# Kernel optimization log

Hardware: AMD Instinct MI355X
Metric: run time of the kernel (lower is better)

## Reference

```python
import jax, jax.numpy as jnp
from jax import lax
import numpy as np

PN_FEAT = 64


def _conv(x, w, b):
    # x: [B,H,W,Cin], w: [kh,kw,Cin,Cout] (SAME padding, stride 1)
    return lax.conv_general_dilated(x, w, (1, 1), 'SAME',
                                    dimension_numbers=('NHWC', 'HWIO', 'NHWC')) + b


def setup_inputs() -> dict:
    key = jax.random.key(0)
    ks = jax.random.split(key, 12)
    B, P, N, C = 4, 5000, 100, 8
    nx = ny = 240
    pillars = jax.random.normal(ks[0], (B, P, N, C), dtype=jnp.float32)
    pillar_idxs = jax.random.randint(ks[1], (B, P, 2), 0, nx).astype(jnp.int32)
    def lin(k, fi, fo):
        return jax.random.normal(k, (fi, fo), dtype=jnp.float32) / np.sqrt(fi).astype(np.float32)
    def cnv(k, kh, kw, ci, co):
        return jax.random.normal(k, (kh, kw, ci, co), dtype=jnp.float32) / np.sqrt(kh * kw * ci).astype(np.float32)
    return {
        'pillars': pillars,
        'pillar_idxs': pillar_idxs,
        'nx': nx,
        'ny': ny,
        # pointnet MLP: 8 -> 64 (tanh) -> 64
        'pn_w0': lin(ks[2], 8, 64), 'pn_b0': jnp.zeros((64,), jnp.float32),
        'pn_w1': lin(ks[3], 64, PN_FEAT), 'pn_b1': jnp.zeros((PN_FEAT,), jnp.float32),
        # resnet costmap CNN: 64 -> 128 (tanh) -> 128 (tanh) -> 1, relu output
        'cw0': cnv(ks[4], 3, 3, PN_FEAT, 128), 'cb0': jnp.zeros((128,), jnp.float32),
        'cw1': cnv(ks[5], 3, 3, 128, 128), 'cb1': jnp.zeros((128,), jnp.float32),
        'cw2': cnv(ks[6], 1, 1, 128, 1), 'cb2': jnp.zeros((1,), jnp.float32),
    }


def reference(pillars, pillar_idxs, nx, ny,
              pn_w0, pn_b0, pn_w1, pn_b1,
              cw0, cb0, cw1, cb1, cw2, cb2):
    VALID_THRESH = 1000000.0
    ACT_SCALE = 1.0
    # mask padded points (norm >= 1e6 means invalid)
    valid = (jnp.linalg.norm(pillars, axis=-1, keepdims=True) < VALID_THRESH).astype(pillars.dtype)
    # per-point MLP: [B,P,N,8] -> [B,P,N,F]
    h = jnp.tanh(pillars @ pn_w0 + pn_b0)
    feat = h @ pn_w1 + pn_b1
    # masked max over points in each pillar -> [B,P,F]
    pmax = jnp.max(feat * valid, axis=-2)
    # scatter pillar features into BEV pseudo-image [B,nx,ny,F]
    B = pillars.shape[0]
    bidx = jnp.arange(B)[:, None]                      # [B,1]
    img = jnp.zeros((B, nx, ny, PN_FEAT), pillars.dtype)
    img = img.at[bidx, pillar_idxs[..., 0], pillar_idxs[..., 1]].set(pmax)
    # costmap CNN head (NHWC internally; original is NCHW, same math)
    x = jnp.tanh(_conv(img, cw0, cb0))
    x = jnp.tanh(_conv(x, cw1, cb1))
    x = _conv(x, cw2, cb2)
    return jax.nn.relu(x) * ACT_SCALE            # [B,nx,ny,1]
```

## Files before the change

### kernel.cpp

```cpp
#include <hip/hip_runtime.h>
#include <hip/hip_bf16.h>
#include <math.h>

#define B  4
#define P  5000
#define NPT 100
#define F  64
#define NX 240
#define NY 240
#define C1 128

typedef __attribute__((ext_vector_type(8)))  short short8;
typedef __attribute__((ext_vector_type(16))) float f32x16;

__device__ __forceinline__ float tanh_fast(float x) {
    float e = exp2f(x * 2.8853900817779268f);
    float r = __builtin_amdgcn_rcpf(e + 1.0f);
    return __builtin_fmaf(-2.0f, r, 1.0f);
}
__device__ __forceinline__ short bf16_bits(float f) {
    return (short)(__bfloat16_as_ushort(__float2bfloat16(f)));
}
__device__ __forceinline__ void async_load16(const void* g, void* l) {
    __builtin_amdgcn_global_load_lds(
        (const __attribute__((address_space(1))) void*)g,
        (__attribute__((address_space(3))) void*)l, 16, 0, 0);
}

__global__ __launch_bounds__(128, 2) void pn_mfma_kernel(
    const float* __restrict__ pillars,
    const short* __restrict__ w0p,
    const __hip_bfloat16* __restrict__ w1t,
    const float* __restrict__ b1,
    const int* __restrict__ idxs,
    const int* __restrict__ winner,
    __hip_bfloat16* __restrict__ img)
{
    constexpr int XS = 40;
    __shared__ short xA[128 * XS];
    __shared__ float red[2][F];
    __shared__ unsigned int vb32[4];

    int bp = blockIdx.x;
    int n  = threadIdx.x;
    int wave = n >> 6, lane = n & 63;
    int mr = lane & 31;
    int g  = lane >> 5;
    bool live = (n < NPT);

    const float* xp = pillars + ((size_t)bp * NPT + (live ? n : 0)) * 8;
    float4 q0 = *(const float4*)xp;
    float4 q1 = *(const float4*)(xp + 4);
    float x[8] = {q0.x, q0.y, q0.z, q0.w, q1.x, q1.y, q1.z, q1.w};

    float ss = 0.f;
#pragma unroll
    for (int c = 0; c < 8; c++) ss += x[c] * x[c];
    bool valid = live && (ss < 1e12f);

    unsigned long long bal = __ballot(valid);
    if (lane == 0) {
        vb32[wave * 2]     = (unsigned)bal;
        vb32[wave * 2 + 1] = (unsigned)(bal >> 32);
    }

    short8 xhi, xlo, xone;
#pragma unroll
    for (int c = 0; c < 8; c++) {
        __hip_bfloat16 hb = __float2bfloat16(x[c]);
        float hv = __bfloat162float(hb);
        xhi[c] = (short)__bfloat16_as_ushort(hb);
        xlo[c] = bf16_bits(x[c] - hv);
        xone[c] = (c < 2) ? bf16_bits(1.0f) : (short)0;
    }
    *(short8*)&xA[n * XS + 0]  = xhi;
    *(short8*)&xA[n * XS + 8]  = xlo;
    *(short8*)&xA[n * XS + 16] = xhi;
    *(short8*)&xA[n * XS + 24] = xone;
    __syncthreads();

    short8 wb[2][2];
#pragma unroll
    for (int kk = 0; kk < 2; kk++)
#pragma unroll
        for (int m = 0; m < 2; m++)
            wb[kk][m] = *(const short8*)(w0p + ((kk * 2 + g) * 64 + m * 32 + mr) * 8);

    f32x16 acc1[2][2];
#pragma unroll
    for (int ptt = 0; ptt < 2; ptt++)
#pragma unroll
        for (int m = 0; m < 2; m++)
            acc1[ptt][m] = (f32x16){0,0,0,0,0,0,0,0,0,0,0,0,0,0,0,0};

#pragma unroll
    for (int kk = 0; kk < 2; kk++) {
        short8 x0 = *(const short8*)&xA[(wave * 64 + mr) * XS + kk * 16 + g * 8];
        short8 x1 = *(const short8*)&xA[(wave * 64 + 32 + mr) * XS + kk * 16 + g * 8];
        acc1[0][0] = __builtin_amdgcn_mfma_f32_32x32x16_bf16(wb[kk][0], x0, acc1[0][0], 0, 0, 0);
        acc1[0][1] = __builtin_amdgcn_mfma_f32_32x32x16_bf16(wb[kk][1], x0, acc1[0][1], 0, 0, 0);
        acc1[1][0] = __builtin_amdgcn_mfma_f32_32x32x16_bf16(wb[kk][0], x1, acc1[1][0], 0, 0, 0);
        acc1[1][1] = __builtin_amdgcn_mfma_f32_32x32x16_bf16(wb[kk][1], x1, acc1[1][1], 0, 0, 0);
    }

    short8 afrag[2][4];
#pragma unroll
    for (int ptt = 0; ptt < 2; ptt++) {
#pragma unroll
        for (int c0 = 0; c0 < 4; c0++) {
            short8 t;
#pragma unroll
            for (int j = 0; j < 8; j++) {
                float v = (c0 >> 1) ? acc1[ptt][1][8 * (c0 & 1) + j]
                                    : acc1[ptt][0][8 * (c0 & 1) + j];
                t[j] = bf16_bits(tanh_fast(v));
            }
            afrag[ptt][c0] = t;
        }
    }

    short8 bfrag[2][4];
#pragma unroll
    for (int nt = 0; nt < 2; nt++)
#pragma unroll
        for (int c0 = 0; c0 < 4; c0++)
            bfrag[nt][c0] = *(const short8*)((const short*)w1t +
                                (nt * 32 + mr) * F + c0 * 16 + g * 8);

    f32x16 a2[2][2];
#pragma unroll
    for (int ptt = 0; ptt < 2; ptt++)
#pragma unroll
        for (int nt = 0; nt < 2; nt++)
            a2[ptt][nt] = (f32x16){0,0,0,0,0,0,0,0,0,0,0,0,0,0,0,0};

#pragma unroll
    for (int c0 = 0; c0 < 4; c0++) {
        a2[0][0] = __builtin_amdgcn_mfma_f32_32x32x16_bf16(afrag[0][c0], bfrag[0][c0], a2[0][0], 0, 0, 0);
        a2[0][1] = __builtin_amdgcn_mfma_f32_32x32x16_bf16(afrag[0][c0], bfrag[1][c0], a2[0][1], 0, 0, 0);
        a2[1][0] = __builtin_amdgcn_mfma_f32_32x32x16_bf16(afrag[1][c0], bfrag[0][c0], a2[1][0], 0, 0, 0);
        a2[1][1] = __builtin_amdgcn_mfma_f32_32x32x16_bf16(afrag[1][c0], bfrag[1][c0], a2[1][1], 0, 0, 0);
    }

    float bv0 = b1[mr];
    float bv1 = b1[32 + mr];
    bool allv = ((vb32[0] & vb32[1] & vb32[2]) == 0xFFFFFFFFu) &&
                ((vb32[3] & 0xFu) == 0xFu);
    float mx0 = -INFINITY, mx1 = -INFINITY;

    if (allv) {
#pragma unroll
        for (int ptt = 0; ptt < 2; ptt++) {
#pragma unroll
            for (int r = 0; r < 16; r++) {
                bool inc = !(wave == 1 && ptt == 1) || (g == 0 && r < 4);
                if (inc) {
                    mx0 = fmaxf(mx0, (ptt == 0) ? a2[0][0][r] : a2[1][0][r]);
                    mx1 = fmaxf(mx1, (ptt == 0) ? a2[0][1][r] : a2[1][1][r]);
                }
            }
        }
        mx0 += bv0;
        mx1 += bv1;
    } else {
        unsigned wm0 = vb32[wave * 2];
        unsigned wm1 = vb32[wave * 2 + 1];
#pragma unroll
        for (int ptt = 0; ptt < 2; ptt++) {
            unsigned wm = (ptt == 0) ? wm0 : wm1;
#pragma unroll
            for (int r = 0; r < 16; r++) {
                int idx = (r & 3) + 8 * (r >> 2) + 4 * g;
                bool inc = !(wave == 1 && ptt == 1) || (idx < 4);
                if (inc) {
                    bool vbit = (wm >> idx) & 1;
                    float a0 = (ptt == 0) ? a2[0][0][r] : a2[1][0][r];
                    float a1 = (ptt == 0) ? a2[0][1][r] : a2[1][1][r];
                    mx0 = fmaxf(mx0, vbit ? (a0 + bv0) : 0.0f);
                    mx1 = fmaxf(mx1, vbit ? (a1 + bv1) : 0.0f);
                }
            }
        }
    }
    mx0 = fmaxf(mx0, __shfl_xor(mx0, 32, 64));
    mx1 = fmaxf(mx1, __shfl_xor(mx1, 32, 64));
    if (lane < 32) { red[wave][mr] = mx0; red[wave][32 + mr] = mx1; }
    __syncthreads();
    if (n < F) {
        float v = fmaxf(red[0][n], red[1][n]);
        int ix = idxs[bp * 2], iy = idxs[bp * 2 + 1];
        int b = bp / P, p = bp % P;
        int cell = (b * NX + ix) * NY + iy;
        if (winner[cell] == p)
            img[(size_t)cell * F + n] = __float2bfloat16(v);
    }
}

__global__ __launch_bounds__(256) void winner_kernel(
    const int* __restrict__ idxs, int* __restrict__ winner)
{
    int i = blockIdx.x * 256 + threadIdx.x;
    if (i >= B * P) return;
    int ix = idxs[i * 2], iy = idxs[i * 2 + 1];
    int b = i / P, p = i % P;
    atomicMax(&winner[(b * NX + ix) * NY + iy], p);
}

__global__ __launch_bounds__(256) void cvt_w_kernel(
    const float* __restrict__ w, __hip_bfloat16* __restrict__ wt, int cin)
{
    int idx = blockIdx.x * 256 + threadIdx.x;
    int total = 9 * cin * 128;
    if (idx >= total) return;
    int co = idx % 128;
    int rest = idx / 128;
    int ci = rest % cin;
    int t  = rest / cin;
    int c0 = ci >> 4, c16 = ci & 15;
    wt[(((size_t)(t * (cin >> 4) + c0)) * 128 + co) * 16 + c16] = __float2bfloat16(w[idx]);
}

__global__ __launch_bounds__(256) void cvt_w1_kernel(
    const float* __restrict__ w1, __hip_bfloat16* __restrict__ w1t)
{
    int idx = blockIdx.x * 256 + threadIdx.x;
    if (idx >= F * F) return;
    int nn = idx >> 6, kk = idx & 63;
    int c0 = kk >> 4, g = (kk >> 3) & 1, j = kk & 7;
    int k = 16 * c0 + 4 * g + (j & 3) + 8 * (j >> 2);
    w1t[nn * F + kk] = __float2bfloat16(w1[k * F + nn]);
}

__global__ __launch_bounds__(256) void cvt_w0p_kernel(
    const float* __restrict__ w0, const float* __restrict__ b0,
    short* __restrict__ w0p)
{
    int idx = blockIdx.x * 256 + threadIdx.x;
    if (idx >= 4 * 64 * 8) return;
    int j = idx & 7;
    int nn = (idx >> 3) & 63;
    int s = idx >> 9;
    short out = 0;
    if (s < 3) {
        float wv = w0[j * F + nn];
        __hip_bfloat16 hb = __float2bfloat16(wv);
        if (s < 2)      out = (short)__bfloat16_as_ushort(hb);
        else            out = bf16_bits(wv - __bfloat162float(hb));
    } else {
        float bv = b0[nn];
        __hip_bfloat16 hb = __float2bfloat16(bv);
        if (j == 0)      out = (short)__bfloat16_as_ushort(hb);
        else if (j == 1) out = bf16_bits(bv - __bfloat162float(hb));
    }
    w0p[idx] = out;
}

template<int CIN, bool FUSE>
__global__ __launch_bounds__(512, 2) void conv_mfma(
    const __hip_bfloat16* __restrict__ in,
    const __hip_bfloat16* __restrict__ wt,
    const float* __restrict__ bias,
    const float* __restrict__ w2,
    const float* __restrict__ b2,
    const __hip_bfloat16* __restrict__ zerobuf,
    __hip_bfloat16* __restrict__ out_bf,
    float* __restrict__ out_f)
{
    constexpr int NPASS = CIN / 32;
    constexpr int NC16  = 2;
    constexpr int CSTR  = 400;
    __shared__ short sP[2][4 * CSTR * 8];
    __shared__ float sred[FUSE ? 2 : 1][4][64];

    int tid  = threadIdx.x;
    int wave = tid >> 6;
    int lane = tid & 63;
    int mr = lane & 31;
    int g  = lane >> 5;
    int coh = wave & 1;
    int xr  = wave >> 1;
    int x0 = blockIdx.x * 4;
    int y0 = blockIdx.y * 62;
    if (y0 > 178) y0 = 178;
    int b  = blockIdx.z;
    int n0 = coh * 64;

    const short* wts = (const short*)wt;

    auto stage = [&](int pp, short* dst) {
        int gy = y0 - 1 + lane;
        bool yok = (gy >= 0 && gy < NY);
#pragma unroll
        for (int j = 0; j < 3; j++) {
            int q  = j * 8 + wave;
            int cc = q & 3;
            int dx = q >> 2;
            int gx = x0 - 1 + dx;
            const __hip_bfloat16* src =
                (yok && gx >= 0 && gx < NX)
                ? &in[(((size_t)b * NX + gx) * NY + gy) * CIN + pp * 32 + cc * 8]
                : zerobuf;
            async_load16(src, (void*)(dst + (cc * CSTR + dx * 64) * 8));
        }
    };

    f32x16 acc[2][2];
#pragma unroll
    for (int mt = 0; mt < 2; mt++)
#pragma unroll
        for (int nt = 0; nt < 2; nt++)
            acc[mt][nt] = (f32x16){0,0,0,0,0,0,0,0,0,0,0,0,0,0,0,0};

    stage(0, sP[0]);

#pragma unroll
    for (int p = 0; p < NPASS; p++) {
        __syncthreads();
        if (p + 1 < NPASS)
            stage(p + 1, sP[(p + 1) & 1]);
        const short* sPb = sP[p & 1];

#pragma unroll
        for (int tap = 0; tap < 9; tap++) {
            int kh = tap / 3, kw = tap % 3;
            int rowcol = (xr + kh) * 64 + kw;
            const short* wrow = wts + ((size_t)(tap * (CIN / 16) + p * NC16) * 128 + n0 + mr) * 16 + g * 8;
#pragma unroll
            for (int c0 = 0; c0 < NC16; c0++) {
                short8 w0f = *(const short8*)(wrow + (size_t)c0 * 2048);
                short8 w1f = *(const short8*)(wrow + (size_t)c0 * 2048 + 512);
                int cc = c0 * 2 + g;
                const short* abase = sPb + (cc * CSTR + rowcol + mr) * 8;
                short8 a0 = *(const short8*)(abase);
                short8 a1 = *(const short8*)(abase + 32 * 8);
                acc[0][0] = __builtin_amdgcn_mfma_f32_32x32x16_bf16(a0, w0f, acc[0][0], 0, 0, 0);
                acc[0][1] = __builtin_amdgcn_mfma_f32_32x32x16_bf16(a0, w1f, acc[0][1], 0, 0, 0);
                acc[1][0] = __builtin_amdgcn_mfma_f32_32x32x16_bf16(a1, w0f, acc[1][0], 0, 0, 0);
                acc[1][1] = __builtin_amdgcn_mfma_f32_32x32x16_bf16(a1, w1f, acc[1][1], 0, 0, 0);
            }
        }
    }

    float bv0 = bias[n0 + mr];
    float bv1 = bias[n0 + 32 + mr];
    if (!FUSE) {
        size_t base = ((size_t)b * NX + (x0 + xr)) * NY;
#pragma unroll
        for (int mt = 0; mt < 2; mt++) {
#pragma unroll
            for (int r = 0; r < 16; r++) {
                int row = mt * 32 + (r & 3) + 8 * (r >> 2) + 4 * g;
                if (row < 62) {
                    int y = y0 + row;
                    out_bf[(base + y) * C1 + n0 + mr]      = __float2bfloat16(tanh_fast(acc[mt][0][r] + bv0));
                    out_bf[(base + y) * C1 + n0 + 32 + mr] = __float2bfloat16(tanh_fast(acc[mt][1][r] + bv1));
                }
            }
        }
    } else {
        float w20 = w2[n0 + mr];
        float w21 = w2[n0 + 32 + mr];
#pragma unroll
        for (int mt = 0; mt < 2; mt++) {
#pragma unroll
            for (int r = 0; r < 16; r++) {
                float v = tanh_fast(acc[mt][0][r] + bv0) * w20
                        + tanh_fast(acc[mt][1][r] + bv1) * w21;
                v += __shfl_xor(v, 1, 64);
                v += __shfl_xor(v, 2, 64);
                v += __shfl_xor(v, 4, 64);
                v += __shfl_xor(v, 8, 64);
                v += __shfl_xor(v, 16, 64);
                if (mr == 0)
                    sred[coh][xr][mt * 32 + (r & 3) + 8 * (r >> 2) + 4 * g] = v;
            }
        }
        __syncthreads();
        if (tid < 256) {
            int xr2 = tid >> 6;
            int yy  = tid & 63;
            if (yy < 62) {
                float r = sred[0][xr2][yy] + sred[1][xr2][yy] + b2[0];
                out_f[((size_t)b * NX + (x0 + xr2)) * NY + (y0 + yy)] = fmaxf(r, 0.f);
            }
        }
    }
}

extern "C" void kernel_launch(void* const* d_in, const int* in_sizes, int n_in,
                              void* d_out, int out_size, void* d_ws, size_t ws_size,
                              hipStream_t stream) {
    const float* pillars = (const float*)d_in[0];
    const int*   idxs    = (const int*)d_in[1];
    const float* pn_w0   = (const float*)d_in[4];
    const float* pn_b0   = (const float*)d_in[5];
    const float* pn_w1   = (const float*)d_in[6];
    const float* pn_b1   = (const float*)d_in[7];
    const float* cw0     = (const float*)d_in[8];
    const float* cb0     = (const float*)d_in[9];
    const float* cw1     = (const float*)d_in[10];
    const float* cb1     = (const float*)d_in[11];
    const float* cw2     = (const float*)d_in[12];
    const float* cb2     = (const float*)d_in[13];
    float* out = (float*)d_out;

    char* ws = (char*)d_ws;
    const size_t IMG_BYTES  = (size_t)B * NX * NY * F * 2;
    const size_t OUT1_BYTES = (size_t)B * NX * NY * C1 * 2;
    const size_t WIN_BYTES  = (size_t)B * NX * NY * 4;
    const size_t PMAX_BYTES = (size_t)B * P * F * 4;
    const size_t WT1_BYTES  = (size_t)9 * C1 * F * 2;
    const size_t WT2_BYTES  = (size_t)9 * C1 * C1 * 2;
    const size_t W1T_BYTES  = (size_t)F * F * 2;
    const size_t W0P_BYTES  = (size_t)4 * 64 * 8 * 2;
    __hip_bfloat16* img  = (__hip_bfloat16*)ws;
    __hip_bfloat16* out1 = (__hip_bfloat16*)(ws + IMG_BYTES);
    int*   winner = (int*)(ws + IMG_BYTES + OUT1_BYTES);
    __hip_bfloat16* wt1 = (__hip_bfloat16*)(ws + IMG_BYTES + OUT1_BYTES + WIN_BYTES + PMAX_BYTES);
    __hip_bfloat16* wt2 = (__hip_bfloat16*)(ws + IMG_BYTES + OUT1_BYTES + WIN_BYTES + PMAX_BYTES + WT1_BYTES);
    __hip_bfloat16* w1t = (__hip_bfloat16*)(ws + IMG_BYTES + OUT1_BYTES + WIN_BYTES + PMAX_BYTES + WT1_BYTES + WT2_BYTES);
    short* w0p = (short*)(ws + IMG_BYTES + OUT1_BYTES + WIN_BYTES + PMAX_BYTES + WT1_BYTES + WT2_BYTES + W1T_BYTES);
    __hip_bfloat16* zerobuf = (__hip_bfloat16*)(ws + IMG_BYTES + OUT1_BYTES + WIN_BYTES + PMAX_BYTES + WT1_BYTES + WT2_BYTES + W1T_BYTES + W0P_BYTES);

    hipMemsetAsync(img, 0, IMG_BYTES, stream);
    hipMemsetAsync(winner, 0xFF, WIN_BYTES, stream);
    hipMemsetAsync(zerobuf, 0, 64, stream);

    cvt_w_kernel<<<(9 * F * C1 + 255) / 256, 256, 0, stream>>>(cw0, wt1, F);
    cvt_w_kernel<<<(9 * C1 * C1 + 255) / 256, 256, 0, stream>>>(cw1, wt2, C1);
    cvt_w1_kernel<<<(F * F + 255) / 256, 256, 0, stream>>>(pn_w1, w1t);
    cvt_w0p_kernel<<<(4 * 64 * 8 + 255) / 256, 256, 0, stream>>>(pn_w0, pn_b0, w0p);

    winner_kernel<<<(B * P + 255) / 256, 256, 0, stream>>>(idxs, winner);
    pn_mfma_kernel<<<B * P, 128, 0, stream>>>(pillars, w0p, w1t, pn_b1,
                                              idxs, winner, img);

    conv_mfma<F, false><<<dim3(NX / 4, 4, B), 512, 0, stream>>>(
        img, wt1, cb0, nullptr, nullptr, zerobuf, out1, nullptr);
    conv_mfma<C1, true><<<dim3(NX / 4, 4, B), 512, 0, stream>>>(
        out1, wt2, cb1, cw2, cb2, zerobuf, nullptr, out);
}
```

Measured before the change: 325.1 us.

## Pad conv activations with y-halo and read A operands directly from global

Stores the BEV image and first conv output with a zero-padded y dimension (248 rows, one halo row before the data), so the convolution kernels no longer need boundary checks in y. The LDS staging with async global-to-LDS loads and the per-pass barriers are removed; each lane instead precomputes nine tap offsets and loads its MFMA A fragments straight from global memory, with out-of-range x rows redirected to a zeroed pad buffer. A small halo kernel zeroes the padding rows of the intermediate buffer. This trades shared-memory reuse across taps for more global/L2 traffic, relying on cache hits to avoid the sync and staging cost.

New measurement: 501.2 us. 1.54x slower.

```diff
diff --git a/kernel.cpp b/kernel.cpp
--- a/kernel.cpp
+++ b/kernel.cpp
@@ -9,6 +9,7 @@
 #define NX 240
 #define NY 240
 #define C1 128
+#define YP 248
 
 typedef __attribute__((ext_vector_type(8)))  short short8;
 typedef __attribute__((ext_vector_type(16))) float f32x16;
@@ -20,11 +21,6 @@
 }
 __device__ __forceinline__ short bf16_bits(float f) {
     return (short)(__bfloat16_as_ushort(__float2bfloat16(f)));
-}
-__device__ __forceinline__ void async_load16(const void* g, void* l) {
-    __builtin_amdgcn_global_load_lds(
-        (const __attribute__((address_space(1))) void*)g,
-        (__attribute__((address_space(3))) void*)l, 16, 0, 0);
 }
 
 __global__ __launch_bounds__(128, 2) void pn_mfma_kernel(
@@ -190,9 +186,8 @@
         float v = fmaxf(red[0][n], red[1][n]);
         int ix = idxs[bp * 2], iy = idxs[bp * 2 + 1];
         int b = bp / P, p = bp % P;
-        int cell = (b * NX + ix) * NY + iy;
-        if (winner[cell] == p)
-            img[(size_t)cell * F + n] = __float2bfloat16(v);
+        if (winner[(b * NX + ix) * NY + iy] == p)
+            img[((size_t)(b * NX + ix) * YP + iy + 1) * F + n] = __float2bfloat16(v);
     }
 }
 
@@ -204,6 +199,20 @@
     int ix = idxs[i * 2], iy = idxs[i * 2 + 1];
     int b = i / P, p = i % P;
     atomicMax(&winner[(b * NX + ix) * NY + iy], p);
+}
+
+__global__ __launch_bounds__(256) void halo_kernel(__hip_bfloat16* __restrict__ out1)
+{
+    int idx = blockIdx.x * 256 + threadIdx.x;
+    if (idx >= B * NX * 4 * (C1 / 8)) return;
+    int c8   = idx & 15;
+    int rest = idx >> 4;
+    int rowi = rest & 3;
+    int rest2 = rest >> 2;
+    int x = rest2 % NX, b = rest2 / NX;
+    int yi = (rowi == 0) ? 0 : (240 + rowi);
+    short8 z = {0,0,0,0,0,0,0,0};
+    *(short8*)&out1[(((size_t)(b * NX + x)) * YP + yi) * C1 + c8 * 8] = z;
 }
 
 __global__ __launch_bounds__(256) void cvt_w_kernel(
@@ -262,14 +271,11 @@
     const float* __restrict__ bias,
     const float* __restrict__ w2,
     const float* __restrict__ b2,
-    const __hip_bfloat16* __restrict__ zerobuf,
+    int zoff,
     __hip_bfloat16* __restrict__ out_bf,
     float* __restrict__ out_f)
 {
     constexpr int NPASS = CIN / 32;
-    constexpr int NC16  = 2;
-    constexpr int CSTR  = 400;
-    __shared__ short sP[2][4 * CSTR * 8];
     __shared__ float sred[FUSE ? 2 : 1][4][64];
 
     int tid  = threadIdx.x;
@@ -285,24 +291,25 @@
     int b  = blockIdx.z;
     int n0 = coh * 64;
 
+    const short* inp = (const short*)in;
     const short* wts = (const short*)wt;
 
-    auto stage = [&](int pp, short* dst) {
-        int gy = y0 - 1 + lane;
-        bool yok = (gy >= 0 && gy < NY);
-#pragma unroll
-        for (int j = 0; j < 3; j++) {
-            int q  = j * 8 + wave;
-            int cc = q & 3;
-            int dx = q >> 2;
-            int gx = x0 - 1 + dx;
-            const __hip_bfloat16* src =
-                (yok && gx >= 0 && gx < NX)
-                ? &in[(((size_t)b * NX + gx) * NY + gy) * CIN + pp * 32 + cc * 8]
-                : zerobuf;
-            async_load16(src, (void*)(dst + (cc * CSTR + dx * 64) * 8));
-        }
-    };
+    int voff[3][3][2];
+#pragma unroll
+    for (int kh = 0; kh < 3; kh++) {
+        int gx = x0 - 1 + xr + kh;
+        bool xok = (gx >= 0 && gx < NX);
+#pragma unroll
+        for (int kw = 0; kw < 3; kw++)
+#pragma unroll
+            for (int mt = 0; mt < 2; mt++) {
+                int yi = y0 + kw + mr + 32 * mt;
+                voff[kh][kw][mt] = xok
+                    ? (((b * NX + gx) * YP + yi) * CIN + g * 8)
+                    : (zoff + lane * 8);
+            }
+    }
+    int wlane = (n0 + mr) * 16 + g * 8;
 
     f32x16 acc[2][2];
 #pragma unroll
@@ -311,28 +318,19 @@
         for (int nt = 0; nt < 2; nt++)
             acc[mt][nt] = (f32x16){0,0,0,0,0,0,0,0,0,0,0,0,0,0,0,0};
 
-    stage(0, sP[0]);
-
 #pragma unroll
     for (int p = 0; p < NPASS; p++) {
-        __syncthreads();
-        if (p + 1 < NPASS)
-            stage(p + 1, sP[(p + 1) & 1]);
-        const short* sPb = sP[p & 1];
-
 #pragma unroll
         for (int tap = 0; tap < 9; tap++) {
-            int kh = tap / 3, kw = tap % 3;
-            int rowcol = (xr + kh) * 64 + kw;
-            const short* wrow = wts + ((size_t)(tap * (CIN / 16) + p * NC16) * 128 + n0 + mr) * 16 + g * 8;
-#pragma unroll
-            for (int c0 = 0; c0 < NC16; c0++) {
-                short8 w0f = *(const short8*)(wrow + (size_t)c0 * 2048);
-                short8 w1f = *(const short8*)(wrow + (size_t)c0 * 2048 + 512);
-                int cc = c0 * 2 + g;
-                const short* abase = sPb + (cc * CSTR + rowcol + mr) * 8;
-                short8 a0 = *(const short8*)(abase);
-                short8 a1 = *(const short8*)(abase + 32 * 8);
+            const int kh = tap / 3, kw = tap % 3;
+#pragma unroll
+            for (int c0 = 0; c0 < 2; c0++) {
+                const int wu  = (tap * (CIN / 16) + p * 2 + c0) * 2048;
+                const int cio = p * 32 + c0 * 16;
+                short8 w0f = *(const short8*)(wts + wu + wlane);
+                short8 w1f = *(const short8*)(wts + wu + wlane + 512);
+                short8 a0  = *(const short8*)(inp + voff[kh][kw][0] + cio);
+                short8 a1  = *(const short8*)(inp + voff[kh][kw][1] + cio);
                 acc[0][0] = __builtin_amdgcn_mfma_f32_32x32x16_bf16(a0, w0f, acc[0][0], 0, 0, 0);
                 acc[0][1] = __builtin_amdgcn_mfma_f32_32x32x16_bf16(a0, w1f, acc[0][1], 0, 0, 0);
                 acc[1][0] = __builtin_amdgcn_mfma_f32_32x32x16_bf16(a1, w0f, acc[1][0], 0, 0, 0);
@@ -344,16 +342,16 @@
     float bv0 = bias[n0 + mr];
     float bv1 = bias[n0 + 32 + mr];
     if (!FUSE) {
-        size_t base = ((size_t)b * NX + (x0 + xr)) * NY;
+        size_t base = ((size_t)b * NX + (x0 + xr)) * YP;
 #pragma unroll
         for (int mt = 0; mt < 2; mt++) {
 #pragma unroll
             for (int r = 0; r < 16; r++) {
                 int row = mt * 32 + (r & 3) + 8 * (r >> 2) + 4 * g;
                 if (row < 62) {
-                    int y = y0 + row;
-                    out_bf[(base + y) * C1 + n0 + mr]      = __float2bfloat16(tanh_fast(acc[mt][0][r] + bv0));
-                    out_bf[(base + y) * C1 + n0 + 32 + mr] = __float2bfloat16(tanh_fast(acc[mt][1][r] + bv1));
+                    int yi = y0 + row + 1;
+                    out_bf[(base + yi) * C1 + n0 + mr]      = __float2bfloat16(tanh_fast(acc[mt][0][r] + bv0));
+                    out_bf[(base + yi) * C1 + n0 + 32 + mr] = __float2bfloat16(tanh_fast(acc[mt][1][r] + bv1));
                 }
             }
         }
@@ -405,10 +403,9 @@
     float* out = (float*)d_out;
 
     char* ws = (char*)d_ws;
-    const size_t IMG_BYTES  = (size_t)B * NX * NY * F * 2;
-    const size_t OUT1_BYTES = (size_t)B * NX * NY * C1 * 2;
+    const size_t IMG_BYTES  = (size_t)B * NX * YP * F * 2;
+    const size_t OUT1_BYTES = (size_t)B * NX * YP * C1 * 2;
     const size_t WIN_BYTES  = (size_t)B * NX * NY * 4;
-    const size_t PMAX_BYTES = (size_t)B * P * F * 4;
     const size_t WT1_BYTES  = (size_t)9 * C1 * F * 2;
     const size_t WT2_BYTES  = (size_t)9 * C1 * C1 * 2;
     const size_t W1T_BYTES  = (size_t)F * F * 2;
@@ -416,27 +413,31 @@
     __hip_bfloat16* img  = (__hip_bfloat16*)ws;
     __hip_bfloat16* out1 = (__hip_bfloat16*)(ws + IMG_BYTES);
     int*   winner = (int*)(ws + IMG_BYTES + OUT1_BYTES);
-    __hip_bfloat16* wt1 = (__hip_bfloat16*)(ws + IMG_BYTES + OUT1_BYTES + WIN_BYTES + PMAX_BYTES);
-    __hip_bfloat16* wt2 = (__hip_bfloat16*)(ws + IMG_BYTES + OUT1_BYTES + WIN_BYTES + PMAX_BYTES + WT1_BYTES);
-    __hip_bfloat16* w1t = (__hip_bfloat16*)(ws + IMG_BYTES + OUT1_BYTES + WIN_BYTES + PMAX_BYTES + WT1_BYTES + WT2_BYTES);
-    short* w0p = (short*)(ws + IMG_BYTES + OUT1_BYTES + WIN_BYTES + PMAX_BYTES + WT1_BYTES + WT2_BYTES + W1T_BYTES);
-    __hip_bfloat16* zerobuf = (__hip_bfloat16*)(ws + IMG_BYTES + OUT1_BYTES + WIN_BYTES + PMAX_BYTES + WT1_BYTES + WT2_BYTES + W1T_BYTES + W0P_BYTES);
+    __hip_bfloat16* wt1 = (__hip_bfloat16*)(ws + IMG_BYTES + OUT1_BYTES + WIN_BYTES);
+    __hip_bfloat16* wt2 = (__hip_bfloat16*)(ws + IMG_BYTES + OUT1_BYTES + WIN_BYTES + WT1_BYTES);
+    __hip_bfloat16* w1t = (__hip_bfloat16*)(ws + IMG_BYTES + OUT1_BYTES + WIN_BYTES + WT1_BYTES + WT2_BYTES);
+    short* w0p = (short*)(ws + IMG_BYTES + OUT1_BYTES + WIN_BYTES + WT1_BYTES + WT2_BYTES + W1T_BYTES);
+    __hip_bfloat16* zeropad = (__hip_bfloat16*)(ws + IMG_BYTES + OUT1_BYTES + WIN_BYTES + WT1_BYTES + WT2_BYTES + W1T_BYTES + W0P_BYTES);
+
+    int zoff1 = (int)((short*)zeropad - (short*)img);
+    int zoff2 = (int)((short*)zeropad - (short*)out1);
 
     hipMemsetAsync(img, 0, IMG_BYTES, stream);
     hipMemsetAsync(winner, 0xFF, WIN_BYTES, stream);
-    hipMemsetAsync(zerobuf, 0, 64, stream);
+    hipMemsetAsync(zeropad, 0, 4096, stream);
 
     cvt_w_kernel<<<(9 * F * C1 + 255) / 256, 256, 0, stream>>>(cw0, wt1, F);
     cvt_w_kernel<<<(9 * C1 * C1 + 255) / 256, 256, 0, stream>>>(cw1, wt2, C1);
     cvt_w1_kernel<<<(F * F + 255) / 256, 256, 0, stream>>>(pn_w1, w1t);
     cvt_w0p_kernel<<<(4 * 64 * 8 + 255) / 256, 256, 0, stream>>>(pn_w0, pn_b0, w0p);
+    halo_kernel<<<(B * NX * 4 * (C1 / 8) + 255) / 256, 256, 0, stream>>>(out1);
 
     winner_kernel<<<(B * P + 255) / 256, 256, 0, stream>>>(idxs, winner);
     pn_mfma_kernel<<<B * P, 128, 0, stream>>>(pillars, w0p, w1t, pn_b1,
                                               idxs, winner, img);
 
     conv_mfma<F, false><<<dim3(NX / 4, 4, B), 512, 0, stream>>>(
-        img, wt1, cb0, nullptr, nullptr, zerobuf, out1, nullptr);
+        img, wt1, cb0, nullptr, nullptr, zoff1, out1, nullptr);
     conv_mfma<C1, true><<<dim3(NX / 4, 4, B), 512, 0, stream>>>(
-        out1, wt2, cb1, cw2, cb2, zerobuf, nullptr, out);
-}
+        out1, wt2, cb1, cw2, cb2, zoff2, nullptr, out);
+}
```
